# Kernel tuning notes

Hardware: AMD Instinct MI355X
Metric: run time of the kernel (lower is better)

Reference implementation:

```python
import jax, jax.numpy as jnp
import numpy as np

HIDDEN = 1024
HEADS = 16
B, L = 2, 2048


def _xavier(key, shape):
    fan_in, fan_out = shape[1], shape[0]
    limit = float(np.sqrt(6.0 / (fan_in + fan_out)))
    return jax.random.uniform(key, shape, jnp.float32, -limit, limit)


def setup_inputs() -> dict:
    key = jax.random.key(0)
    ks = jax.random.split(key, 6)
    return {
        "query": jax.random.normal(ks[0], (B, L, HIDDEN), jnp.float32),
        "bias": jax.random.normal(ks[1], (B, 1, 1, L), jnp.float32),
        "Wq": _xavier(ks[2], (HIDDEN, HIDDEN)), "bq": jnp.zeros((HIDDEN,), jnp.float32),
        "Wk": _xavier(ks[3], (HIDDEN, HIDDEN)), "bk": jnp.zeros((HIDDEN,), jnp.float32),
        "Wv": _xavier(ks[4], (HIDDEN, HIDDEN)), "bv": jnp.zeros((HIDDEN,), jnp.float32),
        "Wo": _xavier(ks[5], (HIDDEN, HIDDEN)), "bo": jnp.zeros((HIDDEN,), jnp.float32),
    }


def _split_heads(x):
    b, l, c = x.shape
    return x.reshape(b, l, HEADS, c // HEADS).transpose(0, 2, 1, 3)  # [B,H,L,d]


def reference(query, bias, Wq, bq, Wk, bk, Wv, bv, Wo, bo):
    d_head = HIDDEN // HEADS
    q = query @ Wq.T + bq
    k = query @ Wk.T + bk
    v = query @ Wv.T + bv
    q = _split_heads(q) * (d_head ** -0.5)  # [B,H,L,d]
    k = _split_heads(k)
    v = _split_heads(v)
    logits = jnp.einsum("bhqd,bhkd->bhqk", q, k) + bias  # [B,H,L,L]
    weights = jax.nn.softmax(logits, axis=-1)
    x = jnp.einsum("bhqk,bhkd->bhqd", weights, v)  # [B,H,L,d]
    x = x.transpose(0, 2, 1, 3).reshape(query.shape[0], query.shape[1], HIDDEN)
    return x @ Wo.T + bo
```

## Files before the change

### kernel.cpp

```cpp
#include <hip/hip_runtime.h>
#include <hip/hip_fp16.h>
#include <stdint.h>

#define HIDDEN 1024
#define HEADS  16
#define DH     64
#define B_     2
#define L_     2048
#define M_TOT  (B_ * L_)
#define ELEMS  (M_TOT * HIDDEN)
#define LOG2E  1.44269504088896340736f

typedef _Float16 f16;
typedef _Float16 f16x4 __attribute__((ext_vector_type(4)));
typedef _Float16 f16x8 __attribute__((ext_vector_type(8)));
typedef float    f32x4 __attribute__((ext_vector_type(4)));
typedef uint32_t u32;
typedef __attribute__((address_space(1))) u32 gu32;
typedef __attribute__((address_space(3))) u32 su32;

#define MFMA32(a, b, c) __builtin_amdgcn_mfma_f32_16x16x32_f16(a, b, c, 0, 0, 0)


__global__ __launch_bounds__(256)
void convert_f16(const float* __restrict__ query,
                 const float* __restrict__ Wq, const float* __restrict__ Wk,
                 const float* __restrict__ Wv, const float* __restrict__ Wo,
                 f16* __restrict__ Qh, f16* __restrict__ Wh)
{
    const int NQ4 = ELEMS / 4;
    const int NW4 = (HIDDEN * HIDDEN) / 4;
    const int total = NQ4 + 4 * NW4;
    for (int u = blockIdx.x * 256 + threadIdx.x; u < total; u += gridDim.x * 256) {
        float4 v; f16* dp;
        if (u < NQ4) {
            v = ((const float4*)query)[u];
            dp = Qh + (size_t)u * 4;
        } else {
            const int u2 = u - NQ4;
            const int w = u2 >> 18;
            const int off = u2 & (NW4 - 1);
            const float* W = (w == 0) ? Wq : (w == 1) ? Wk : (w == 2) ? Wv : Wo;
            v = ((const float4*)W)[off];
            dp = Wh + (size_t)u2 * 4;
        }
        f16x4 h = { (f16)v.x, (f16)v.y, (f16)v.z, (f16)v.w };
        *(f16x4*)dp = h;
    }
}

template<int TM, int TN>
__device__ __forceinline__
void gemm_loop(const f16* __restrict__ A, const f16* __restrict__ W,
               int mb, int nb, f32x4 (&acc)[TM / 32][TN / 32])
{
    __shared__ f16 As[2][TM * 32];
    __shared__ f16 Bs[2][TN * 32];

    const int tid  = threadIdx.x;
    const int lane = tid & 63;
    const int wave = tid >> 6;
    const int quad = lane >> 4;
    const int l16  = lane & 15;
    const int wm   = (wave >> 1) * (TM / 2);
    const int wn   = (wave & 1) * (TN / 2);

    constexpr int AISS = TM / 64;
    constexpr int BISS = TN / 64;
    int aoff[AISS], boff[BISS];
#pragma unroll
    for (int q = 0; q < AISS; q++) {
        const int p16 = (wave * AISS + q) * 64 + lane;
        const int r = p16 >> 2;
        const int c8 = (p16 & 3) ^ ((r >> 1) & 3);
        aoff[q] = (mb + r) * HIDDEN + c8 * 8;
    }
#pragma unroll
    for (int q = 0; q < BISS; q++) {
        const int p16 = (wave * BISS + q) * 64 + lane;
        const int r = p16 >> 2;
        const int c8 = (p16 & 3) ^ ((r >> 1) & 3);
        boff[q] = (nb + r) * HIDDEN + c8 * 8;
    }

#pragma unroll
    for (int q = 0; q < AISS; q++)
        __builtin_amdgcn_global_load_lds((gu32*)&A[aoff[q]],
                                         (su32*)&As[0][(wave * AISS + q) * 512], 16, 0, 0);
#pragma unroll
    for (int q = 0; q < BISS; q++)
        __builtin_amdgcn_global_load_lds((gu32*)&W[boff[q]],
                                         (su32*)&Bs[0][(wave * BISS + q) * 512], 16, 0, 0);
    __syncthreads();

    for (int kb = 0; kb < HIDDEN; kb += 32) {
        const int buf = (kb >> 5) & 1;
        const int nkb = (kb + 32 < HIDDEN) ? kb + 32 : 0;

#pragma unroll
        for (int q = 0; q < AISS; q++)
            __builtin_amdgcn_global_load_lds((gu32*)&A[aoff[q] + nkb],
                                             (su32*)&As[buf ^ 1][(wave * AISS + q) * 512], 16, 0, 0);
#pragma unroll
        for (int q = 0; q < BISS; q++)
            __builtin_amdgcn_global_load_lds((gu32*)&W[boff[q] + nkb],
                                             (su32*)&Bs[buf ^ 1][(wave * BISS + q) * 512], 16, 0, 0);

        f16x8 af[TM / 32], bf[TN / 32];
#pragma unroll
        for (int i = 0; i < TM / 32; i++) {
            const int r = wm + i * 16 + l16;
            af[i] = *(const f16x8*)&As[buf][r * 32 + (quad ^ ((r >> 1) & 3)) * 8];
        }
#pragma unroll
        for (int j = 0; j < TN / 32; j++) {
            const int r = wn + j * 16 + l16;
            bf[j] = *(const f16x8*)&Bs[buf][r * 32 + (quad ^ ((r >> 1) & 3)) * 8];
        }
#pragma unroll
        for (int i = 0; i < TM / 32; i++)
#pragma unroll
            for (int j = 0; j < TN / 32; j++)
                acc[i][j] = MFMA32(af[i], bf[j], acc[i][j]);
        __syncthreads();
    }
}

__global__ __launch_bounds__(256)
void proj_qkv(const f16* __restrict__ A, const f16* __restrict__ W,
              const float* __restrict__ bq, const float* __restrict__ bk,
              const float* __restrict__ bv,
              f16* __restrict__ Qo, f16* __restrict__ Ko, f16* __restrict__ Vo)
{
    f32x4 acc[4][4] = {};
    const int mb = blockIdx.x * 128, nb = blockIdx.y * 128;
    gemm_loop<128, 128>(A, W, mb, nb, acc);

    const int lane = threadIdx.x & 63, wave = threadIdx.x >> 6;
    const int quad = lane >> 4, l16 = lane & 15;
    const int wm = (wave >> 1) * 64, wn = (wave & 1) * 64;
    const int nsel = nb >> 10;
    const int nbase = nb & 1023;

    if (nsel < 2) {
        const float* bias = nsel ? bk : bq;
        f16* out = nsel ? Ko : Qo;
        const float scale = nsel ? 1.0f : 0.125f * LOG2E;
#pragma unroll
        for (int i = 0; i < 4; i++)
#pragma unroll
            for (int j = 0; j < 4; j++) {
                const int n1 = nbase + wn + j * 16 + l16;
                const float bn = bias[n1];
                const int h = n1 >> 6, dd = n1 & 63;
#pragma unroll
                for (int r = 0; r < 4; r++) {
                    const int m = mb + wm + i * 16 + quad * 4 + r;
                    const int b = m >> 11, l = m & (L_ - 1);
                    out[(((b * HEADS + h) * L_) + l) * DH + dd] =
                        (f16)((acc[i][j][r] + bn) * scale);
                }
            }
    } else {
#pragma unroll
        for (int i = 0; i < 4; i++)
#pragma unroll
            for (int j = 0; j < 4; j++) {
                const int n1 = nbase + wn + j * 16 + l16;
                const float bn = bv[n1];
                const int h = n1 >> 6, dd = n1 & 63;
                const int m0 = mb + wm + i * 16 + quad * 4;
                const int b = m0 >> 11, l0 = m0 & (L_ - 1);
                f16x4 pk;
#pragma unroll
                for (int r = 0; r < 4; r++) pk[r] = (f16)(acc[i][j][r] + bn);
                *(f16x4*)&Vo[((size_t)(b * HEADS + h) * DH + dd) * L_ + l0] = pk;
            }
    }
}

__global__ __launch_bounds__(256)
void proj_out(const f16* __restrict__ A, const f16* __restrict__ W,
              const float* __restrict__ bo, float* __restrict__ out)
{
    f32x4 acc[4][2] = {};
    const int mb = blockIdx.x * 128, nb = blockIdx.y * 64;
    gemm_loop<128, 64>(A, W, mb, nb, acc);

    const int lane = threadIdx.x & 63, wave = threadIdx.x >> 6;
    const int quad = lane >> 4, l16 = lane & 15;
    const int wm = (wave >> 1) * 64, wn = (wave & 1) * 32;
#pragma unroll
    for (int i = 0; i < 4; i++)
#pragma unroll
        for (int j = 0; j < 2; j++) {
            const int n = nb + wn + j * 16 + l16;
            const float bn = bo[n];
#pragma unroll
            for (int r = 0; r < 4; r++) {
                const int m = mb + wm + i * 16 + quad * 4 + r;
                out[m * HIDDEN + n] = acc[i][j][r] + bn;
            }
        }
}

__global__ __launch_bounds__(256)
void attn(const f16* __restrict__ Q, const f16* __restrict__ K,
          const f16* __restrict__ Vt, const float* __restrict__ bias,
          f16* __restrict__ X)
{
    __shared__ f16 Ks[2][64 * 64];
    __shared__ f16 Vs[2][64 * 64];
    __shared__ float biasl[L_];

    const int tid  = threadIdx.x;
    const int lane = tid & 63;
    const int wave = tid >> 6;
    const int quad = lane >> 4;
    const int l16  = lane & 15;

    const int bid = (int)blockIdx.x;
    const int lb  = (bid & 7) * 128 + (bid >> 3);
    const int bh = lb >> 5;
    const int b  = bh >> 4, h = bh & 15;
    const int qrow0 = (lb & 31) * 64 + wave * 16;

    const f16* Qh  = Q  + (size_t)bh * L_ * DH;
    const f16* Kh  = K  + (size_t)bh * L_ * DH;
    const f16* Vth = Vt + (size_t)bh * DH * L_;

    {
        const float4* bb = (const float4*)(bias + b * L_);
        for (int i = tid; i < L_ / 4; i += 256) {
            const float4 v = bb[i];
            biasl[i * 4 + 0] = v.x * LOG2E;
            biasl[i * 4 + 1] = v.y * LOG2E;
            biasl[i * 4 + 2] = v.z * LOG2E;
            biasl[i * 4 + 3] = v.w * LOG2E;
        }
    }

    int krow[2], kcol[2], vcol[2];
#pragma unroll
    for (int q = 0; q < 2; q++) {
        const int p = (wave * 2 + q) * 64 + lane;
        const int r = p >> 3;
        const int w = p & 7;
        krow[q] = r;
        kcol[q] = (w ^ (r & 7) ^ (((r >> 3) & 1) << 2)) * 8;
        vcol[q] = (w ^ (r & 7)) * 8;
    }

    f16x8 qf[2];
#pragma unroll
    for (int hh = 0; hh < 2; hh++)
        qf[hh] = *(const f16x8*)&Qh[(qrow0 + l16) * DH + hh * 32 + quad * 8];

    int koffX[2][2], koffY[2][2], voff[2][4];
#pragma unroll
    for (int g = 0; g < 2; g++) {
        const int rX = g * 32 + ((l16 >> 2) << 3) + (l16 & 3);
        const int rY = rX + 4;
        const int gkX = (rX & 7) ^ (((rX >> 3) & 1) << 2);
        const int gkY = (rY & 7) ^ (((rY >> 3) & 1) << 2);
#pragma unroll
        for (int hh = 0; hh < 2; hh++) {
            koffX[g][hh] = rX * 64 + (((hh * 4 + quad) ^ gkX) << 3);
            koffY[g][hh] = rY * 64 + (((hh * 4 + quad) ^ gkY) << 3);
        }
#pragma unroll
        for (int t = 0; t < 4; t++) {
            const int vr = t * 16 + l16;
            voff[g][t] = vr * 64 + (((g * 4 + quad) ^ (vr & 7)) << 3);
        }
    }

#pragma unroll
    for (int q = 0; q < 2; q++) {
        __builtin_amdgcn_global_load_lds((gu32*)(Kh + (size_t)krow[q] * DH + kcol[q]),
                                         (su32*)&Ks[0][(wave * 2 + q) * 512], 16, 0, 0);
        __builtin_amdgcn_global_load_lds((gu32*)(Vth + (size_t)krow[q] * L_ + vcol[q]),
                                         (su32*)&Vs[0][(wave * 2 + q) * 512], 16, 0, 0);
    }

    f32x4 o[4] = {};
    f32x4 osum = {};
    const f16x8 ones8 = { (f16)1.f, (f16)1.f, (f16)1.f, (f16)1.f,
                          (f16)1.f, (f16)1.f, (f16)1.f, (f16)1.f };
    __syncthreads();

#pragma unroll 1
    for (int kb = 0; kb < L_; kb += 64) {
        const int buf = (kb >> 6) & 1;
        const int nkb = (kb + 64 < L_) ? kb + 64 : 0;

#pragma unroll
        for (int q = 0; q < 2; q++) {
            __builtin_amdgcn_global_load_lds(
                (gu32*)(Kh + (size_t)(nkb + krow[q]) * DH + kcol[q]),
                (su32*)&Ks[buf ^ 1][(wave * 2 + q) * 512], 16, 0, 0);
            __builtin_amdgcn_global_load_lds(
                (gu32*)(Vth + (size_t)krow[q] * L_ + nkb + vcol[q]),
                (su32*)&Vs[buf ^ 1][(wave * 2 + q) * 512], 16, 0, 0);
        }

#pragma unroll
        for (int g = 0; g < 2; g++) {
            const f16x8 kx0 = *(const f16x8*)&Ks[buf][koffX[g][0]];
            const f16x8 kx1 = *(const f16x8*)&Ks[buf][koffX[g][1]];
            const f16x8 ky0 = *(const f16x8*)&Ks[buf][koffY[g][0]];
            const f16x8 ky1 = *(const f16x8*)&Ks[buf][koffY[g][1]];
            f16x8 va[4];
#pragma unroll
            for (int t = 0; t < 4; t++)
                va[t] = *(const f16x8*)&Vs[buf][voff[g][t]];
            const f32x4 blvX = *(const f32x4*)&biasl[kb + g * 32 + quad * 8];
            const f32x4 blvY = *(const f32x4*)&biasl[kb + g * 32 + quad * 8 + 4];

            f32x4 zx = blvX, zy = blvY;
            zx = MFMA32(kx0, qf[0], zx);
            zx = MFMA32(kx1, qf[1], zx);
            zy = MFMA32(ky0, qf[0], zy);
            zy = MFMA32(ky1, qf[1], zy);
            const f16x8 pb = {
                (f16)__builtin_amdgcn_exp2f(zx[0]), (f16)__builtin_amdgcn_exp2f(zx[1]),
                (f16)__builtin_amdgcn_exp2f(zx[2]), (f16)__builtin_amdgcn_exp2f(zx[3]),
                (f16)__builtin_amdgcn_exp2f(zy[0]), (f16)__builtin_amdgcn_exp2f(zy[1]),
                (f16)__builtin_amdgcn_exp2f(zy[2]), (f16)__builtin_amdgcn_exp2f(zy[3]) };
#pragma unroll
            for (int t = 0; t < 4; t++)
                o[t] = MFMA32(va[t], pb, o[t]);
            osum = MFMA32(ones8, pb, osum);
        }
        __syncthreads();
    }

    {
        const float inv = 1.0f / osum[0];
        const size_t qrow = (size_t)b * L_ + qrow0 + l16;
#pragma unroll
        for (int t = 0; t < 4; t++) {
            f16x4 pk;
#pragma unroll
            for (int r = 0; r < 4; r++) pk[r] = (f16)(o[t][r] * inv);
            *(f16x4*)&X[qrow * HIDDEN + h * DH + t * 16 + quad * 4] = pk;
        }
    }
}

extern "C" void kernel_launch(void* const* d_in, const int* in_sizes, int n_in,
                              void* d_out, int out_size, void* d_ws, size_t ws_size,
                              hipStream_t stream)
{
    const float* query = (const float*)d_in[0];
    const float* bias  = (const float*)d_in[1];
    const float* Wq = (const float*)d_in[2]; const float* bq = (const float*)d_in[3];
    const float* Wk = (const float*)d_in[4]; const float* bk = (const float*)d_in[5];
    const float* Wv = (const float*)d_in[6]; const float* bv = (const float*)d_in[7];
    const float* Wo = (const float*)d_in[8]; const float* bo = (const float*)d_in[9];
    float* out = (float*)d_out;

    f16* Wh = (f16*)d_ws;
    f16* Qh = Wh + 4096 * 1024;
    f16* Kf = Qh + ELEMS;
    f16* Vf = Kf + ELEMS;
    f16* Qf = Vf + ELEMS;
    f16* Xf = Qh;

    convert_f16<<<2048, 256, 0, stream>>>(query, Wq, Wk, Wv, Wo, Qh, Wh);
    proj_qkv<<<dim3(32, 24), 256, 0, stream>>>(Qh, Wh, bq, bk, bv, Qf, Kf, Vf);
    attn<<<1024, 256, 0, stream>>>(Qf, Kf, Vf, bias, Xf);
    proj_out<<<dim3(32, 16), 256, 0, stream>>>(Xf, Wh + 3072 * 1024, bo, out);
}
```

Baseline: 201.8 us.

## Triple-buffer GEMM LDS tiles with one barrier per k-step and vmcnt waits

After: 201.4 us. About the same (-0.2%).

```diff
diff --git a/kernel.cpp b/kernel.cpp
--- a/kernel.cpp
+++ b/kernel.cpp
@@ -54,8 +54,8 @@
 void gemm_loop(const f16* __restrict__ A, const f16* __restrict__ W,
                int mb, int nb, f32x4 (&acc)[TM / 32][TN / 32])
 {
-    __shared__ f16 As[2][TM * 32];
-    __shared__ f16 Bs[2][TN * 32];
+    __shared__ f16 As[3][TM * 32];
+    __shared__ f16 Bs[3][TN * 32];
 
     const int tid  = threadIdx.x;
     const int lane = tid & 63;
@@ -84,46 +84,58 @@
     }
 
 #pragma unroll
-    for (int q = 0; q < AISS; q++)
-        __builtin_amdgcn_global_load_lds((gu32*)&A[aoff[q]],
-                                         (su32*)&As[0][(wave * AISS + q) * 512], 16, 0, 0);
-#pragma unroll
-    for (int q = 0; q < BISS; q++)
-        __builtin_amdgcn_global_load_lds((gu32*)&W[boff[q]],
-                                         (su32*)&Bs[0][(wave * BISS + q) * 512], 16, 0, 0);
-    __syncthreads();
-
+    for (int p = 0; p < 2; p++) {
+#pragma unroll
+        for (int q = 0; q < AISS; q++)
+            __builtin_amdgcn_global_load_lds((gu32*)&A[aoff[q] + p * 32],
+                                             (su32*)&As[p][(wave * AISS + q) * 512], 16, 0, 0);
+#pragma unroll
+        for (int q = 0; q < BISS; q++)
+            __builtin_amdgcn_global_load_lds((gu32*)&W[boff[q] + p * 32],
+                                             (su32*)&Bs[p][(wave * BISS + q) * 512], 16, 0, 0);
+    }
+
+    int sl = 0;
+#pragma unroll 1
     for (int kb = 0; kb < HIDDEN; kb += 32) {
-        const int buf = (kb >> 5) & 1;
-        const int nkb = (kb + 32 < HIDDEN) ? kb + 32 : 0;
-
+        if constexpr (AISS + BISS == 4)
+            asm volatile("s_waitcnt vmcnt(4)" ::: "memory");
+        else
+            asm volatile("s_waitcnt vmcnt(3)" ::: "memory");
+        __builtin_amdgcn_s_barrier();
+        __builtin_amdgcn_sched_barrier(0);
+
+        const int nkb = (kb + 64 < HIDDEN) ? kb + 64 : 0;
+        const int si  = (sl >= 1) ? sl - 1 : 2;
 #pragma unroll
         for (int q = 0; q < AISS; q++)
             __builtin_amdgcn_global_load_lds((gu32*)&A[aoff[q] + nkb],
-                                             (su32*)&As[buf ^ 1][(wave * AISS + q) * 512], 16, 0, 0);
+                                             (su32*)&As[si][(wave * AISS + q) * 512], 16, 0, 0);
 #pragma unroll
         for (int q = 0; q < BISS; q++)
             __builtin_amdgcn_global_load_lds((gu32*)&W[boff[q] + nkb],
-                                             (su32*)&Bs[buf ^ 1][(wave * BISS + q) * 512], 16, 0, 0);
+                                             (su32*)&Bs[si][(wave * BISS + q) * 512], 16, 0, 0);
 
         f16x8 af[TM / 32], bf[TN / 32];
 #pragma unroll
         for (int i = 0; i < TM / 32; i++) {
             const int r = wm + i * 16 + l16;
-            af[i] = *(const f16x8*)&As[buf][r * 32 + (quad ^ ((r >> 1) & 3)) * 8];
+            af[i] = *(const f16x8*)&As[sl][r * 32 + (quad ^ ((r >> 1) & 3)) * 8];
         }
 #pragma unroll
         for (int j = 0; j < TN / 32; j++) {
             const int r = wn + j * 16 + l16;
-            bf[j] = *(const f16x8*)&Bs[buf][r * 32 + (quad ^ ((r >> 1) & 3)) * 8];
+            bf[j] = *(const f16x8*)&Bs[sl][r * 32 + (quad ^ ((r >> 1) & 3)) * 8];
         }
 #pragma unroll
         for (int i = 0; i < TM / 32; i++)
 #pragma unroll
             for (int j = 0; j < TN / 32; j++)
                 acc[i][j] = MFMA32(af[i], bf[j], acc[i][j]);
-        __syncthreads();
-    }
+
+        sl = (sl + 1 == 3) ? 0 : sl + 1;
+    }
+    asm volatile("s_waitcnt vmcnt(0)" ::: "memory");
 }
 
 __global__ __launch_bounds__(256)
```
